# Performance work log

Measured on AMD Instinct MI355X. Metric: run time of the kernel, lower is better.

Reference implementation:

```python
import jax, jax.numpy as jnp
import numpy as np

BITS = 4
GROUPSIZE = 128
IN_FEATURES = 4096
OUT_FEATURES = 11008
PACK = 32 // BITS  # 8 nibbles per int32
MASK = (1 << BITS) - 1


def setup_inputs() -> dict:
    key = jax.random.key(0)
    k_x, k_qw, k_qz, k_s, k_b = jax.random.split(key, 5)
    n_groups = IN_FEATURES // GROUPSIZE  # 32
    x = jax.random.normal(k_x, (2, 2048, IN_FEATURES), dtype=jnp.float32)
    # packed int32 buffers: random bit patterns (each int32 holds 8 4-bit values)
    qweight = jax.random.randint(k_qw, (IN_FEATURES // 32 * BITS, OUT_FEATURES),
                                 -2**31, 2**31 - 1, dtype=jnp.int32)
    qzeros = jax.random.randint(k_qz, (n_groups, OUT_FEATURES // 32 * BITS),
                                -2**31, 2**31 - 1, dtype=jnp.int32)
    scales = jax.random.uniform(k_s, (n_groups, OUT_FEATURES), dtype=jnp.float32,
                                minval=0.001, maxval=0.02)
    bias = jax.random.normal(k_b, (OUT_FEATURES,), dtype=jnp.float32) * 0.01
    return {"x": x, "qweight": qweight, "scales": scales, "qzeros": qzeros, "bias": bias}


def _dequant(qweight, scales, qzeros):
    # shift amounts for each packed nibble: [0,4,...,28]
    wf = jnp.arange(0, 32, BITS, dtype=jnp.int32)
    n_groups = scales.shape[0]
    # unpack zeros: [G, out//8] -> [G, out//8, 8] -> [G, 1, out]
    zeros = jnp.bitwise_and(jnp.right_shift(qzeros[:, :, None], wf[None, None, :]), MASK)
    zeros = zeros.reshape(n_groups, 1, OUT_FEATURES).astype(scales.dtype)
    # unpack weights: [in//8, out] -> [in//8, 8, out] -> [G, groupsize, out]
    w = jnp.bitwise_and(jnp.right_shift(qweight[:, None, :], wf[None, :, None]), MASK)
    w = w.reshape(n_groups, GROUPSIZE, OUT_FEATURES).astype(scales.dtype)
    sc = scales[:, None, :]  # [G, 1, out]
    weight = sc * w - sc * zeros  # scales*w - scale_zeros
    return weight.reshape(IN_FEATURES, OUT_FEATURES)


def reference(x, qweight, scales, qzeros, bias):
    weight = _dequant(qweight, scales, qzeros)
    return jnp.matmul(x, weight) + bias
```

## Files before the change

### kernel.cpp

```cpp
#include <hip/hip_runtime.h>
#include <cstdint>
#include <cstddef>

#define IN_F 4096
#define OUT_F 11008
#define M_ROWS 4096
#define QZ_STRIDE (OUT_F / 8)
#define NKT (IN_F / 128)
#define NGROUPS 32

typedef __attribute__((ext_vector_type(4))) float f32x4;
typedef __attribute__((ext_vector_type(4))) int i32x4;
typedef __attribute__((ext_vector_type(8))) __bf16 bf16x8;
typedef uint32_t u32;
typedef uint16_t u16;
typedef uint8_t u8;

__device__ __forceinline__ u16 f2bf(float f) {
  u32 u = __builtin_bit_cast(u32, f);
  u += 0x7FFFu + ((u >> 16) & 1u);
  return (u16)(u >> 16);
}

__global__ __launch_bounds__(256) void conv_x_i8(const float* __restrict__ x,
                                                 u8* __restrict__ xq,
                                                 float* __restrict__ xs) {
  const int row = blockIdx.x;
  const int tid = threadIdx.x;
  const float* xr = x + (size_t)row * IN_F;
  float4 v[4];
#pragma unroll
  for (int j = 0; j < 4; ++j)
    v[j] = reinterpret_cast<const float4*>(xr)[tid * 4 + j];
  float am = 0.f;
#pragma unroll
  for (int j = 0; j < 4; ++j)
    am = fmaxf(am, fmaxf(fmaxf(fabsf(v[j].x), fabsf(v[j].y)),
                         fmaxf(fabsf(v[j].z), fabsf(v[j].w))));
#pragma unroll
  for (int off = 32; off > 0; off >>= 1) am = fmaxf(am, __shfl_xor(am, off, 64));
  __shared__ float wmax[4];
  if ((tid & 63) == 0) wmax[tid >> 6] = am;
  __syncthreads();
  am = fmaxf(fmaxf(wmax[0], wmax[1]), fmaxf(wmax[2], wmax[3]));
  const float amc = fmaxf(am, 1e-30f);
  const float inv = 127.f / amc;
  if (tid == 0) xs[row] = amc / 127.f;
  u32 o[4];
#pragma unroll
  for (int j = 0; j < 4; ++j) {
    u32 b0 = (u32)(u8)(int8_t)__float2int_rn(v[j].x * inv);
    u32 b1 = (u32)(u8)(int8_t)__float2int_rn(v[j].y * inv);
    u32 b2 = (u32)(u8)(int8_t)__float2int_rn(v[j].z * inv);
    u32 b3 = (u32)(u8)(int8_t)__float2int_rn(v[j].w * inv);
    o[j] = b0 | (b1 << 8) | (b2 << 16) | (b3 << 24);
  }
  *reinterpret_cast<uint4*>(xq + (size_t)row * IN_F + tid * 16) =
      make_uint4(o[0], o[1], o[2], o[3]);
}

__global__ void colscale_kernel(const float* __restrict__ scl,
                                float* __restrict__ Scol,
                                float* __restrict__ invScol) {
  const int n = blockIdx.x * 256 + threadIdx.x;
  if (n >= OUT_F) return;
  float m = 0.f;
#pragma unroll 4
  for (int g = 0; g < NGROUPS; ++g) m = fmaxf(m, scl[(size_t)g * OUT_F + n]);
  const float S = m * (15.f / 127.f);
  Scol[n] = S;
  invScol[n] = 1.f / S;
}

__global__ void dequant_i8(const int* __restrict__ qw, const int* __restrict__ qz,
                           const float* __restrict__ scl,
                           const float* __restrict__ invScol,
                           u8* __restrict__ wq8) {
  const int nl = threadIdx.x & 31, rl = threadIdx.x >> 5;
  const int n = blockIdx.x * 32 + nl;
  const int r = blockIdx.y * 8 + rl;
  const int g = r >> 4;
  u32 q = (u32)qw[(size_t)r * OUT_F + n];
  const int z = (int)(((u32)qz[g * QZ_STRIDE + (n >> 3)] >> (4 * (n & 7))) & 15u);
  const float si = scl[(size_t)g * OUT_F + n] * invScol[n];
  u32 lo = 0, hi = 0;
#pragma unroll
  for (int e = 0; e < 4; ++e) {
    float f = fminf(fmaxf((float)((int)((q >> (4 * e)) & 15u) - z) * si, -127.f), 127.f);
    lo |= ((u32)(u8)(int8_t)__float2int_rn(f)) << (8 * e);
  }
#pragma unroll
  for (int e = 0; e < 4; ++e) {
    float f = fminf(fmaxf((float)((int)((q >> (16 + 4 * e)) & 15u) - z) * si, -127.f), 127.f);
    hi |= ((u32)(u8)(int8_t)__float2int_rn(f)) << (8 * e);
  }
  *reinterpret_cast<uint2*>(wq8 + (size_t)n * IN_F + r * 8) = make_uint2(lo, hi);
}

__global__ __launch_bounds__(512, 2) void gemm256_i8(
    const u8* __restrict__ xq, const u8* __restrict__ wq,
    const float* __restrict__ Scol, const float* __restrict__ xs,
    const float* __restrict__ bias, float* __restrict__ out) {
  __shared__ __align__(16) u8 As[2][256 * 128];
  __shared__ __align__(16) u8 Bs[2][256 * 128];
  const int tid = threadIdx.x;
  const int lane = tid & 63, wid = tid >> 6;
  const int cpx = (int)gridDim.x >> 3;
  const int swz = ((int)blockIdx.x & 7) * cpx + ((int)blockIdx.x >> 3);
  const int m0 = (swz & 15) * 256, n0 = (swz >> 4) * 256;
  const int wr = wid >> 2, wc = wid & 3;
  const int frow = lane & 15, q4 = lane >> 4, f7 = lane & 7;
  const int lrow = lane >> 3, ls = lane & 7;

  const int colb0 = ((q4 ^ f7) << 4);
  const int colb1 = (((4 | q4) ^ f7) << 4);
  const int arowB = (wr * 128 + frow) * 128;
  const int browB = (wc * 64 + frow) * 128;

  const u8* gA = xq + (size_t)(m0 + lrow) * IN_F + ((ls ^ lrow) << 4);
  const u8* gB = wq + (size_t)(n0 + lrow) * IN_F + ((ls ^ lrow) << 4);
  const int rsbase = (wid >> 2) * 128 + (wid & 3) * 16;

  i32x4 acc[8][4] = {};
  i32x4 af[4][2], ah[4][2], bf[4][2];

  auto stage = [&](u8* ldsb, const u8* gl, int u, int h) {
#pragma unroll
    for (int j = 0; j < 2; ++j) {
      const int rowstart = rsbase + j * 8 + h * 64;
      __builtin_amdgcn_global_load_lds(
          (__attribute__((address_space(1))) void*)(gl + (size_t)rowstart * IN_F + (size_t)u * 128),
          (__attribute__((address_space(3))) void*)(ldsb + rowstart * 128), 16, 0, 0);
    }
  };

  stage(Bs[0], gB, 0, 0);
  stage(Bs[0], gB, 0, 1);
  stage(As[0], gA, 0, 0);
  stage(As[0], gA, 0, 1);
  stage(Bs[1], gB, 1, 0);
  stage(Bs[1], gB, 1, 1);
  stage(As[1], gA, 1, 0);
  stage(As[1], gA, 1, 1);
  asm volatile("s_waitcnt vmcnt(8)" ::: "memory");
  __builtin_amdgcn_s_barrier();
  {
    const u8* Ac = As[0];
    const u8* Bc = Bs[0];
#pragma unroll
    for (int ni = 0; ni < 4; ++ni) {
      bf[ni][0] = *reinterpret_cast<const i32x4*>(Bc + browB + ni * 2048 + colb0);
      bf[ni][1] = *reinterpret_cast<const i32x4*>(Bc + browB + ni * 2048 + colb1);
    }
#pragma unroll
    for (int mi = 0; mi < 4; ++mi) {
      af[mi][0] = *reinterpret_cast<const i32x4*>(Ac + arowB + mi * 2048 + colb0);
      af[mi][1] = *reinterpret_cast<const i32x4*>(Ac + arowB + mi * 2048 + colb1);
    }
  }

  for (int u = 0; u < NKT; ++u) {
    const int cur = u & 1;
    const u8* Ac = As[cur];
    const u8* An = As[cur ^ 1];
    const u8* Bn = Bs[cur ^ 1];
    const bool stT = (u + 2 < NKT);

    __builtin_amdgcn_s_barrier();
    asm volatile("s_waitcnt lgkmcnt(0)" ::: "memory");
    __builtin_amdgcn_sched_barrier(0);
    __builtin_amdgcn_s_setprio(1);
#pragma unroll
    for (int mi = 0; mi < 4; ++mi)
#pragma unroll
      for (int ni = 0; ni < 4; ++ni) {
        acc[mi][ni] = __builtin_amdgcn_mfma_i32_16x16x64_i8(af[mi][0], bf[ni][0], acc[mi][ni], 0, 0, 0);
        acc[mi][ni] = __builtin_amdgcn_mfma_i32_16x16x64_i8(af[mi][1], bf[ni][1], acc[mi][ni], 0, 0, 0);
      }
    __builtin_amdgcn_s_setprio(0);
    if (stT) {
      stage(Bs[cur], gB, u + 2, 0);
      stage(Bs[cur], gB, u + 2, 1);
    }
#pragma unroll
    for (int mi = 0; mi < 4; ++mi) {
      ah[mi][0] = *reinterpret_cast<const i32x4*>(Ac + arowB + (4 + mi) * 2048 + colb0);
      ah[mi][1] = *reinterpret_cast<const i32x4*>(Ac + arowB + (4 + mi) * 2048 + colb1);
    }

    __builtin_amdgcn_s_barrier();
    asm volatile("s_waitcnt lgkmcnt(0)" ::: "memory");
    __builtin_amdgcn_sched_barrier(0);
    __builtin_amdgcn_s_setprio(1);
#pragma unroll
    for (int mi = 0; mi < 4; ++mi)
#pragma unroll
      for (int ni = 0; ni < 4; ++ni) {
        acc[4 + mi][ni] = __builtin_amdgcn_mfma_i32_16x16x64_i8(ah[mi][0], bf[ni][0], acc[4 + mi][ni], 0, 0, 0);
        acc[4 + mi][ni] = __builtin_amdgcn_mfma_i32_16x16x64_i8(ah[mi][1], bf[ni][1], acc[4 + mi][ni], 0, 0, 0);
      }
    __builtin_amdgcn_s_setprio(0);
    if (stT) {
      stage(As[cur], gA, u + 2, 0);
      stage(As[cur], gA, u + 2, 1);
    }
    if (stT)
      asm volatile("s_waitcnt vmcnt(8)" ::: "memory");
    else
      asm volatile("s_waitcnt vmcnt(0)" ::: "memory");
    if (u + 1 < NKT) {
#pragma unroll
      for (int ni = 0; ni < 4; ++ni) {
        bf[ni][0] = *reinterpret_cast<const i32x4*>(Bn + browB + ni * 2048 + colb0);
        bf[ni][1] = *reinterpret_cast<const i32x4*>(Bn + browB + ni * 2048 + colb1);
      }
#pragma unroll
      for (int mi = 0; mi < 4; ++mi) {
        af[mi][0] = *reinterpret_cast<const i32x4*>(An + arowB + mi * 2048 + colb0);
        af[mi][1] = *reinterpret_cast<const i32x4*>(An + arowB + mi * 2048 + colb1);
      }
    }
  }

  const int crow = (lane >> 4) * 4, ccol = lane & 15;
#pragma unroll
  for (int mi = 0; mi < 8; ++mi) {
    const int rowb = m0 + wr * 128 + mi * 16 + crow;
    float sxv[4];
#pragma unroll
    for (int r2 = 0; r2 < 4; ++r2) sxv[r2] = xs[rowb + r2];
#pragma unroll
    for (int ni = 0; ni < 4; ++ni) {
      const int col = n0 + wc * 64 + ni * 16 + ccol;
      const float bv = bias[col];
      const float sv = Scol[col];
#pragma unroll
      for (int r2 = 0; r2 < 4; ++r2)
        __builtin_nontemporal_store(
            fmaf(sxv[r2] * sv, (float)acc[mi][ni][r2], bv),
            out + (size_t)(rowb + r2) * OUT_F + col);
    }
  }
}

__global__ __launch_bounds__(256, 2) void gemm_fused(
    const float* __restrict__ x, const int* __restrict__ qw,
    const int* __restrict__ qz, const float* __restrict__ sc,
    const float* __restrict__ bias, float* __restrict__ out) {
  __shared__ u16 Asb[128 * 64];
  __shared__ u16 Bsb[128 * 64];
  const int tid = threadIdx.x;
  const int lane = tid & 63, wid = tid >> 6;
  const int bm = blockIdx.x & 31, bn = blockIdx.x >> 5;
  const int m0 = bm * 128, n0 = bn * 128;
  const int wr = wid >> 1, wc = wid & 1;
  const int frow = lane & 15, fk = (lane >> 4) * 8;
  f32x4 acc[4][4] = {};

  for (int kt = 0; kt < 64; ++kt) {
    const int k0 = kt * 64;
#pragma unroll
    for (int it = 0; it < 8; ++it) {
      int c = it * 256 + tid;
      int row = c >> 4, c4 = c & 15;
      float4 v = *reinterpret_cast<const float4*>(
          x + (size_t)(m0 + row) * IN_F + k0 + c4 * 4);
      uint2 o;
      o.x = (u32)f2bf(v.x) | ((u32)f2bf(v.y) << 16);
      o.y = (u32)f2bf(v.z) | ((u32)f2bf(v.w) << 16);
      *reinterpret_cast<uint2*>(Asb + row * 64 + c4 * 4) = o;
    }
    {
      int nl = tid & 127, rq = tid >> 7;
      int n = n0 + nl;
      int gq = k0 >> 7;
      int z = (int)(((u32)qz[gq * QZ_STRIDE + (n >> 3)] >> (4 * (n & 7))) & 15u);
      float s = sc[gq * OUT_F + n];
#pragma unroll
      for (int j = 0; j < 4; ++j) {
        int r = (k0 >> 3) + rq * 4 + j;
        u32 q = (u32)qw[(size_t)r * OUT_F + n];
        u32 o[4];
#pragma unroll
        for (int e = 0; e < 4; ++e) {
          u16 lo = f2bf(s * (float)((int)((q >> (8 * e)) & 15u) - z));
          u16 hi = f2bf(s * (float)((int)((q >> (8 * e + 4)) & 15u) - z));
          o[e] = (u32)lo | ((u32)hi << 16);
        }
        *reinterpret_cast<uint4*>(Bsb + nl * 64 + (rq * 4 + j) * 8) =
            make_uint4(o[0], o[1], o[2], o[3]);
      }
    }
    __syncthreads();
#pragma unroll
    for (int kk = 0; kk < 64; kk += 32) {
      bf16x8 a[4], b[4];
#pragma unroll
      for (int mi = 0; mi < 4; ++mi)
        a[mi] = *reinterpret_cast<const bf16x8*>(Asb + (wr * 64 + mi * 16 + frow) * 64 + kk + fk);
#pragma unroll
      for (int ni = 0; ni < 4; ++ni)
        b[ni] = *reinterpret_cast<const bf16x8*>(Bsb + (wc * 64 + ni * 16 + frow) * 64 + kk + fk);
#pragma unroll
      for (int mi = 0; mi < 4; ++mi)
#pragma unroll
        for (int ni = 0; ni < 4; ++ni)
          acc[mi][ni] = __builtin_amdgcn_mfma_f32_16x16x32_bf16(a[mi], b[ni], acc[mi][ni], 0, 0, 0);
    }
    __syncthreads();
  }
  const int crow = (lane >> 4) * 4, ccol = lane & 15;
#pragma unroll
  for (int mi = 0; mi < 4; ++mi) {
#pragma unroll
    for (int ni = 0; ni < 4; ++ni) {
      int col = n0 + wc * 64 + ni * 16 + ccol;
      float bv = bias[col];
      int rowb = m0 + wr * 64 + mi * 16 + crow;
#pragma unroll
      for (int r2 = 0; r2 < 4; ++r2)
        out[(size_t)(rowb + r2) * OUT_F + col] = acc[mi][ni][r2] + bv;
    }
  }
}

extern "C" void kernel_launch(void* const* d_in, const int* in_sizes, int n_in,
                              void* d_out, int out_size, void* d_ws, size_t ws_size,
                              hipStream_t stream) {
  const float* x = (const float*)d_in[0];
  const int* qw = (const int*)d_in[1];
  const float* sc = (const float*)d_in[2];
  const int* qz = (const int*)d_in[3];
  const float* bias = (const float*)d_in[4];
  float* out = (float*)d_out;

  const size_t xq_bytes = (size_t)M_ROWS * IN_F;
  const size_t wq_bytes = (size_t)OUT_F * IN_F;
  const size_t xs_bytes = (size_t)M_ROWS * 4;
  const size_t sc_bytes = (size_t)OUT_F * 4;

  if (ws_size >= xq_bytes + wq_bytes + xs_bytes + 2 * sc_bytes) {
    u8* xqp = (u8*)d_ws;
    u8* wqp = (u8*)d_ws + xq_bytes;
    float* xsp = (float*)((u8*)d_ws + xq_bytes + wq_bytes);
    float* Scolp = (float*)((u8*)d_ws + xq_bytes + wq_bytes + xs_bytes);
    float* invScolp = Scolp + OUT_F;
    hipLaunchKernelGGL(conv_x_i8, dim3(M_ROWS), dim3(256), 0, stream, x, xqp, xsp);
    hipLaunchKernelGGL(colscale_kernel, dim3((OUT_F + 255) / 256), dim3(256), 0,
                       stream, sc, Scolp, invScolp);
    hipLaunchKernelGGL(dequant_i8, dim3(OUT_F / 32, 512 / 8), dim3(256), 0,
                       stream, qw, qz, sc, invScolp, wqp);
    hipLaunchKernelGGL(gemm256_i8, dim3((M_ROWS / 256) * (OUT_F / 256)),
                       dim3(512), 0, stream, xqp, wqp, Scolp, xsp, bias, out);
  } else {
    hipLaunchKernelGGL(gemm_fused, dim3(32 * 86), dim3(256), 0, stream, x, qw,
                       qz, sc, bias, out);
  }
}
```

Measured before the change: 248.8 us.

## Split int8 GEMM main loop into eight barrier-synchronized quadrant phases

Restructures the gemm256_i8 K-loop into eight small phases. Each phase runs one 2x2 quadrant of MFMAs, with LDS fragment reads and global-to-LDS prefetches interleaved between phases. Fragment registers shrink from full A/B sets to two small ping-pong buffers, and global pointers are precomputed and incremented instead of recomputed. The aim is finer overlap of LDS traffic, async loads and MFMA work, plus lower register pressure. The cost is many more barriers and waitcnt points per iteration, which can serialize the waves.

```diff
diff --git a/kernel.cpp b/kernel.cpp
--- a/kernel.cpp
+++ b/kernel.cpp
@@ -96,6 +96,48 @@
   }
   *reinterpret_cast<uint2*>(wq8 + (size_t)n * IN_F + r * 8) = make_uint2(lo, hi);
 }
+
+#define SP1 __builtin_amdgcn_s_setprio(1)
+#define SP0 __builtin_amdgcn_s_setprio(0)
+#define BAR __builtin_amdgcn_s_barrier()
+#define PH_SYNC()                                      \
+  __builtin_amdgcn_s_barrier();                        \
+  asm volatile("s_waitcnt lgkmcnt(0)" ::: "memory");   \
+  __builtin_amdgcn_sched_barrier(0)
+
+#define READ_A(ab, pair, base)                                                                  \
+  do {                                                                                          \
+    afr[ab][0][0] = *reinterpret_cast<const i32x4*>((base) + arowB + (2 * (pair)) * 2048 + colb0); \
+    afr[ab][0][1] = *reinterpret_cast<const i32x4*>((base) + arowB + (2 * (pair)) * 2048 + colb1); \
+    afr[ab][1][0] = *reinterpret_cast<const i32x4*>((base) + arowB + (2 * (pair) + 1) * 2048 + colb0); \
+    afr[ab][1][1] = *reinterpret_cast<const i32x4*>((base) + arowB + (2 * (pair) + 1) * 2048 + colb1); \
+  } while (0)
+
+#define READ_B(np, base)                                                                        \
+  do {                                                                                          \
+    bfr[np][0][0] = *reinterpret_cast<const i32x4*>((base) + browB + (2 * (np)) * 2048 + colb0); \
+    bfr[np][0][1] = *reinterpret_cast<const i32x4*>((base) + browB + (2 * (np)) * 2048 + colb1); \
+    bfr[np][1][0] = *reinterpret_cast<const i32x4*>((base) + browB + (2 * (np) + 1) * 2048 + colb0); \
+    bfr[np][1][1] = *reinterpret_cast<const i32x4*>((base) + browB + (2 * (np) + 1) * 2048 + colb1); \
+  } while (0)
+
+#define MFMA_Q(mp, np, ab)                                                                      \
+  do {                                                                                          \
+    SP1;                                                                                        \
+    _Pragma("unroll") for (int m = 0; m < 2; ++m)                                               \
+        _Pragma("unroll") for (int n = 0; n < 2; ++n) {                                         \
+      acc[2 * (mp) + m][2 * (np) + n] = __builtin_amdgcn_mfma_i32_16x16x64_i8(                  \
+          afr[ab][m][0], bfr[np][n][0], acc[2 * (mp) + m][2 * (np) + n], 0, 0, 0);              \
+      acc[2 * (mp) + m][2 * (np) + n] = __builtin_amdgcn_mfma_i32_16x16x64_i8(                  \
+          afr[ab][m][1], bfr[np][n][1], acc[2 * (mp) + m][2 * (np) + n], 0, 0, 0);              \
+    }                                                                                           \
+    SP0;                                                                                        \
+  } while (0)
+
+#define GLDS(gp, ldsoff)                                                            \
+  __builtin_amdgcn_global_load_lds(                                                 \
+      (__attribute__((address_space(1))) void*)(gp),                                \
+      (__attribute__((address_space(3))) void*)(ldsoff), 16, 0, 0)
 
 __global__ __launch_bounds__(512, 2) void gemm256_i8(
     const u8* __restrict__ xq, const u8* __restrict__ wq,
@@ -120,17 +162,17 @@
   const u8* gA = xq + (size_t)(m0 + lrow) * IN_F + ((ls ^ lrow) << 4);
   const u8* gB = wq + (size_t)(n0 + lrow) * IN_F + ((ls ^ lrow) << 4);
   const int rsbase = (wid >> 2) * 128 + (wid & 3) * 16;
+  const int r0 = rsbase, r1 = rsbase + 8, r2 = rsbase + 64, r3 = rsbase + 72;
+  const int o0 = r0 * 128, o1 = r1 * 128, o2 = r2 * 128, o3 = r3 * 128;
 
   i32x4 acc[8][4] = {};
-  i32x4 af[4][2], ah[4][2], bf[4][2];
+  i32x4 afr[2][2][2], bfr[2][2][2];
 
   auto stage = [&](u8* ldsb, const u8* gl, int u, int h) {
 #pragma unroll
     for (int j = 0; j < 2; ++j) {
       const int rowstart = rsbase + j * 8 + h * 64;
-      __builtin_amdgcn_global_load_lds(
-          (__attribute__((address_space(1))) void*)(gl + (size_t)rowstart * IN_F + (size_t)u * 128),
-          (__attribute__((address_space(3))) void*)(ldsb + rowstart * 128), 16, 0, 0);
+      GLDS(gl + (size_t)rowstart * IN_F + (size_t)u * 128, ldsb + rowstart * 128);
     }
   };
 
@@ -144,82 +186,78 @@
   stage(As[1], gA, 1, 1);
   asm volatile("s_waitcnt vmcnt(8)" ::: "memory");
   __builtin_amdgcn_s_barrier();
-  {
-    const u8* Ac = As[0];
-    const u8* Bc = Bs[0];
-#pragma unroll
-    for (int ni = 0; ni < 4; ++ni) {
-      bf[ni][0] = *reinterpret_cast<const i32x4*>(Bc + browB + ni * 2048 + colb0);
-      bf[ni][1] = *reinterpret_cast<const i32x4*>(Bc + browB + ni * 2048 + colb1);
-    }
-#pragma unroll
-    for (int mi = 0; mi < 4; ++mi) {
-      af[mi][0] = *reinterpret_cast<const i32x4*>(Ac + arowB + mi * 2048 + colb0);
-      af[mi][1] = *reinterpret_cast<const i32x4*>(Ac + arowB + mi * 2048 + colb1);
-    }
-  }
+  READ_A(0, 0, (const u8*)As[0]);
+  READ_B(0, (const u8*)Bs[0]);
+
+  const u8* pA0 = gA + (size_t)r0 * IN_F + 256;
+  const u8* pA1 = gA + (size_t)r1 * IN_F + 256;
+  const u8* pA2 = gA + (size_t)r2 * IN_F + 256;
+  const u8* pA3 = gA + (size_t)r3 * IN_F + 256;
+  const u8* pB0 = gB + (size_t)r0 * IN_F + 256;
+  const u8* pB1 = gB + (size_t)r1 * IN_F + 256;
+  const u8* pB2 = gB + (size_t)r2 * IN_F + 256;
+  const u8* pB3 = gB + (size_t)r3 * IN_F + 256;
 
   for (int u = 0; u < NKT; ++u) {
     const int cur = u & 1;
-    const u8* Ac = As[cur];
-    const u8* An = As[cur ^ 1];
-    const u8* Bn = Bs[cur ^ 1];
+    const u8* Ac = (const u8*)As[cur];
+    const u8* Bc = (const u8*)Bs[cur];
+    const u8* An = (const u8*)As[cur ^ 1];
+    const u8* Bn = (const u8*)Bs[cur ^ 1];
+    u8* Ast = (u8*)As[cur];
+    u8* Bst = (u8*)Bs[cur];
     const bool stT = (u + 2 < NKT);
 
-    __builtin_amdgcn_s_barrier();
-    asm volatile("s_waitcnt lgkmcnt(0)" ::: "memory");
-    __builtin_amdgcn_sched_barrier(0);
-    __builtin_amdgcn_s_setprio(1);
-#pragma unroll
-    for (int mi = 0; mi < 4; ++mi)
-#pragma unroll
-      for (int ni = 0; ni < 4; ++ni) {
-        acc[mi][ni] = __builtin_amdgcn_mfma_i32_16x16x64_i8(af[mi][0], bf[ni][0], acc[mi][ni], 0, 0, 0);
-        acc[mi][ni] = __builtin_amdgcn_mfma_i32_16x16x64_i8(af[mi][1], bf[ni][1], acc[mi][ni], 0, 0, 0);
-      }
-    __builtin_amdgcn_s_setprio(0);
-    if (stT) {
-      stage(Bs[cur], gB, u + 2, 0);
-      stage(Bs[cur], gB, u + 2, 1);
-    }
-#pragma unroll
-    for (int mi = 0; mi < 4; ++mi) {
-      ah[mi][0] = *reinterpret_cast<const i32x4*>(Ac + arowB + (4 + mi) * 2048 + colb0);
-      ah[mi][1] = *reinterpret_cast<const i32x4*>(Ac + arowB + (4 + mi) * 2048 + colb1);
-    }
-
-    __builtin_amdgcn_s_barrier();
-    asm volatile("s_waitcnt lgkmcnt(0)" ::: "memory");
-    __builtin_amdgcn_sched_barrier(0);
-    __builtin_amdgcn_s_setprio(1);
-#pragma unroll
-    for (int mi = 0; mi < 4; ++mi)
-#pragma unroll
-      for (int ni = 0; ni < 4; ++ni) {
-        acc[4 + mi][ni] = __builtin_amdgcn_mfma_i32_16x16x64_i8(ah[mi][0], bf[ni][0], acc[4 + mi][ni], 0, 0, 0);
-        acc[4 + mi][ni] = __builtin_amdgcn_mfma_i32_16x16x64_i8(ah[mi][1], bf[ni][1], acc[4 + mi][ni], 0, 0, 0);
-      }
-    __builtin_amdgcn_s_setprio(0);
-    if (stT) {
-      stage(As[cur], gA, u + 2, 0);
-      stage(As[cur], gA, u + 2, 1);
-    }
+    READ_B(1, Bc);
+    PH_SYNC();
+    MFMA_Q(0, 0, 0);
+    BAR;
+
+    READ_A(1, 1, Ac);
+    PH_SYNC();
+    MFMA_Q(0, 1, 0);
+    BAR;
+
+    if (stT) { GLDS(pB0, Bst + o0); GLDS(pB1, Bst + o1); }
+    PH_SYNC();
+    MFMA_Q(1, 1, 1);
+    BAR;
+
+    READ_A(0, 2, Ac);
+    if (stT) { GLDS(pB2, Bst + o2); GLDS(pB3, Bst + o3); }
+    PH_SYNC();
+    MFMA_Q(1, 0, 1);
+    BAR;
+
+    READ_A(1, 3, Ac);
+    PH_SYNC();
+    MFMA_Q(2, 0, 0);
+    BAR;
+
+    if (stT) { GLDS(pA0, Ast + o0); GLDS(pA1, Ast + o1); }
+    PH_SYNC();
+    MFMA_Q(2, 1, 0);
+    BAR;
+
+    if (stT) { GLDS(pA2, Ast + o2); GLDS(pA3, Ast + o3); }
+    PH_SYNC();
+    MFMA_Q(3, 0, 1);
+    BAR;
+
     if (stT)
       asm volatile("s_waitcnt vmcnt(8)" ::: "memory");
     else
       asm volatile("s_waitcnt vmcnt(0)" ::: "memory");
     if (u + 1 < NKT) {
-#pragma unroll
-      for (int ni = 0; ni < 4; ++ni) {
-        bf[ni][0] = *reinterpret_cast<const i32x4*>(Bn + browB + ni * 2048 + colb0);
-        bf[ni][1] = *reinterpret_cast<const i32x4*>(Bn + browB + ni * 2048 + colb1);
-      }
-#pragma unroll
-      for (int mi = 0; mi < 4; ++mi) {
-        af[mi][0] = *reinterpret_cast<const i32x4*>(An + arowB + mi * 2048 + colb0);
-        af[mi][1] = *reinterpret_cast<const i32x4*>(An + arowB + mi * 2048 + colb1);
-      }
-    }
+      READ_A(0, 0, An);
+      READ_B(0, Bn);
+    }
+    PH_SYNC();
+    MFMA_Q(3, 1, 1);
+    BAR;
+
+    pA0 += 128; pA1 += 128; pA2 += 128; pA3 += 128;
+    pB0 += 128; pB1 += 128; pB2 += 128; pB3 += 128;
   }
 
   const int crow = (lane >> 4) * 4, ccol = lane & 15;
@@ -228,17 +266,17 @@
     const int rowb = m0 + wr * 128 + mi * 16 + crow;
     float sxv[4];
 #pragma unroll
-    for (int r2 = 0; r2 < 4; ++r2) sxv[r2] = xs[rowb + r2];
+    for (int r5 = 0; r5 < 4; ++r5) sxv[r5] = xs[rowb + r5];
 #pragma unroll
     for (int ni = 0; ni < 4; ++ni) {
       const int col = n0 + wc * 64 + ni * 16 + ccol;
       const float bv = bias[col];
       const float sv = Scol[col];
 #pragma unroll
-      for (int r2 = 0; r2 < 4; ++r2)
+      for (int r5 = 0; r5 < 4; ++r5)
         __builtin_nontemporal_store(
-            fmaf(sxv[r2] * sv, (float)acc[mi][ni][r2], bv),
-            out + (size_t)(rowb + r2) * OUT_F + col);
+            fmaf(sxv[r5] * sv, (float)acc[mi][ni][r5], bv),
+            out + (size_t)(rowb + r5) * OUT_F + col);
     }
   }
 }
@@ -318,8 +356,8 @@
       float bv = bias[col];
       int rowb = m0 + wr * 64 + mi * 16 + crow;
 #pragma unroll
-      for (int r2 = 0; r2 < 4; ++r2)
-        out[(size_t)(rowb + r2) * OUT_F + col] = acc[mi][ni][r2] + bv;
+      for (int r5 = 0; r5 < 4; ++r5)
+        out[(size_t)(rowb + r5) * OUT_F + col] = acc[mi][ni][r5] + bv;
     }
   }
 }
```

Result: slower. 261.5 us (+5.1%).

## Pre-swizzle int8 operands into MFMA fragment layout and load straight to registers

Applied to the files above, without the earlier changes.

The quantize and dequant kernels now write x and the weights in a tiled layout that matches the MFMA 16x64 fragment order. The GEMM drops shared memory and the global_load_lds staging, and each wave loads fragments directly from global memory into registers, with double-buffered register sets. The block tile shrinks from 256x256 to 256x128 and each wave computes a 64x64 tile. This removes LDS traffic and barriers, but operands are no longer shared through LDS, so more global/L2 traffic is redundant and there is less reuse per block.

```diff
diff --git a/kernel.cpp b/kernel.cpp
--- a/kernel.cpp
+++ b/kernel.cpp
@@ -8,6 +8,7 @@
 #define QZ_STRIDE (OUT_F / 8)
 #define NKT (IN_F / 128)
 #define NGROUPS 32
+#define KC (IN_F / 64)
 
 typedef __attribute__((ext_vector_type(4))) float f32x4;
 typedef __attribute__((ext_vector_type(4))) int i32x4;
@@ -23,7 +24,7 @@
 }
 
 __global__ __launch_bounds__(256) void conv_x_i8(const float* __restrict__ x,
-                                                 u8* __restrict__ xq,
+                                                 u8* __restrict__ xqf,
                                                  float* __restrict__ xs) {
   const int row = blockIdx.x;
   const int tid = threadIdx.x;
@@ -55,8 +56,10 @@
     u32 b3 = (u32)(u8)(int8_t)__float2int_rn(v[j].w * inv);
     o[j] = b0 | (b1 << 8) | (b2 << 16) | (b3 << 24);
   }
-  *reinterpret_cast<uint4*>(xq + (size_t)row * IN_F + tid * 16) =
-      make_uint4(o[0], o[1], o[2], o[3]);
+  const int k0 = tid * 16;
+  u8* dst = xqf + ((size_t)(row >> 4) * KC + (k0 >> 6)) * 1024 +
+            (size_t)(((row & 15) + (((k0 >> 4) & 3) << 4)) * 16);
+  *reinterpret_cast<uint4*>(dst) = make_uint4(o[0], o[1], o[2], o[3]);
 }
 
 __global__ void colscale_kernel(const float* __restrict__ scl,
@@ -75,7 +78,7 @@
 __global__ void dequant_i8(const int* __restrict__ qw, const int* __restrict__ qz,
                            const float* __restrict__ scl,
                            const float* __restrict__ invScol,
-                           u8* __restrict__ wq8) {
+                           u8* __restrict__ wqf) {
   const int nl = threadIdx.x & 31, rl = threadIdx.x >> 5;
   const int n = blockIdx.x * 32 + nl;
   const int r = blockIdx.y * 8 + rl;
@@ -94,138 +97,74 @@
     float f = fminf(fmaxf((float)((int)((q >> (16 + 4 * e)) & 15u) - z) * si, -127.f), 127.f);
     hi |= ((u32)(u8)(int8_t)__float2int_rn(f)) << (8 * e);
   }
-  *reinterpret_cast<uint2*>(wq8 + (size_t)n * IN_F + r * 8) = make_uint2(lo, hi);
-}
-
-__global__ __launch_bounds__(512, 2) void gemm256_i8(
-    const u8* __restrict__ xq, const u8* __restrict__ wq,
+  const int k0 = r * 8;
+  u8* dst = wqf + ((size_t)(n >> 4) * KC + (k0 >> 6)) * 1024 +
+            (size_t)(((n & 15) + (((k0 >> 4) & 3) << 4)) * 16) + (k0 & 8);
+  *reinterpret_cast<uint2*>(dst) = make_uint2(lo, hi);
+}
+
+__global__ __launch_bounds__(512, 2) void gemm_reg_i8(
+    const u8* __restrict__ xqf, const u8* __restrict__ wqf,
     const float* __restrict__ Scol, const float* __restrict__ xs,
     const float* __restrict__ bias, float* __restrict__ out) {
-  __shared__ __align__(16) u8 As[2][256 * 128];
-  __shared__ __align__(16) u8 Bs[2][256 * 128];
   const int tid = threadIdx.x;
   const int lane = tid & 63, wid = tid >> 6;
   const int cpx = (int)gridDim.x >> 3;
   const int swz = ((int)blockIdx.x & 7) * cpx + ((int)blockIdx.x >> 3);
-  const int m0 = (swz & 15) * 256, n0 = (swz >> 4) * 256;
-  const int wr = wid >> 2, wc = wid & 3;
-  const int frow = lane & 15, q4 = lane >> 4, f7 = lane & 7;
-  const int lrow = lane >> 3, ls = lane & 7;
-
-  const int colb0 = ((q4 ^ f7) << 4);
-  const int colb1 = (((4 | q4) ^ f7) << 4);
-  const int arowB = (wr * 128 + frow) * 128;
-  const int browB = (wc * 64 + frow) * 128;
-
-  const u8* gA = xq + (size_t)(m0 + lrow) * IN_F + ((ls ^ lrow) << 4);
-  const u8* gB = wq + (size_t)(n0 + lrow) * IN_F + ((ls ^ lrow) << 4);
-  const int rsbase = (wid >> 2) * 128 + (wid & 3) * 16;
-
-  i32x4 acc[8][4] = {};
-  i32x4 af[4][2], ah[4][2], bf[4][2];
-
-  auto stage = [&](u8* ldsb, const u8* gl, int u, int h) {
-#pragma unroll
-    for (int j = 0; j < 2; ++j) {
-      const int rowstart = rsbase + j * 8 + h * 64;
-      __builtin_amdgcn_global_load_lds(
-          (__attribute__((address_space(1))) void*)(gl + (size_t)rowstart * IN_F + (size_t)u * 128),
-          (__attribute__((address_space(3))) void*)(ldsb + rowstart * 128), 16, 0, 0);
-    }
-  };
-
-  stage(Bs[0], gB, 0, 0);
-  stage(Bs[0], gB, 0, 1);
-  stage(As[0], gA, 0, 0);
-  stage(As[0], gA, 0, 1);
-  stage(Bs[1], gB, 1, 0);
-  stage(Bs[1], gB, 1, 1);
-  stage(As[1], gA, 1, 0);
-  stage(As[1], gA, 1, 1);
-  asm volatile("s_waitcnt vmcnt(8)" ::: "memory");
-  __builtin_amdgcn_s_barrier();
-  {
-    const u8* Ac = As[0];
-    const u8* Bc = Bs[0];
-#pragma unroll
-    for (int ni = 0; ni < 4; ++ni) {
-      bf[ni][0] = *reinterpret_cast<const i32x4*>(Bc + browB + ni * 2048 + colb0);
-      bf[ni][1] = *reinterpret_cast<const i32x4*>(Bc + browB + ni * 2048 + colb1);
-    }
-#pragma unroll
-    for (int mi = 0; mi < 4; ++mi) {
-      af[mi][0] = *reinterpret_cast<const i32x4*>(Ac + arowB + mi * 2048 + colb0);
-      af[mi][1] = *reinterpret_cast<const i32x4*>(Ac + arowB + mi * 2048 + colb1);
-    }
-  }
-
-  for (int u = 0; u < NKT; ++u) {
-    const int cur = u & 1;
-    const u8* Ac = As[cur];
-    const u8* An = As[cur ^ 1];
-    const u8* Bn = Bs[cur ^ 1];
-    const bool stT = (u + 2 < NKT);
-
-    __builtin_amdgcn_s_barrier();
-    asm volatile("s_waitcnt lgkmcnt(0)" ::: "memory");
-    __builtin_amdgcn_sched_barrier(0);
-    __builtin_amdgcn_s_setprio(1);
-#pragma unroll
-    for (int mi = 0; mi < 4; ++mi)
-#pragma unroll
-      for (int ni = 0; ni < 4; ++ni) {
-        acc[mi][ni] = __builtin_amdgcn_mfma_i32_16x16x64_i8(af[mi][0], bf[ni][0], acc[mi][ni], 0, 0, 0);
-        acc[mi][ni] = __builtin_amdgcn_mfma_i32_16x16x64_i8(af[mi][1], bf[ni][1], acc[mi][ni], 0, 0, 0);
-      }
-    __builtin_amdgcn_s_setprio(0);
-    if (stT) {
-      stage(Bs[cur], gB, u + 2, 0);
-      stage(Bs[cur], gB, u + 2, 1);
-    }
-#pragma unroll
-    for (int mi = 0; mi < 4; ++mi) {
-      ah[mi][0] = *reinterpret_cast<const i32x4*>(Ac + arowB + (4 + mi) * 2048 + colb0);
-      ah[mi][1] = *reinterpret_cast<const i32x4*>(Ac + arowB + (4 + mi) * 2048 + colb1);
-    }
-
-    __builtin_amdgcn_s_barrier();
-    asm volatile("s_waitcnt lgkmcnt(0)" ::: "memory");
-    __builtin_amdgcn_sched_barrier(0);
-    __builtin_amdgcn_s_setprio(1);
-#pragma unroll
-    for (int mi = 0; mi < 4; ++mi)
-#pragma unroll
-      for (int ni = 0; ni < 4; ++ni) {
-        acc[4 + mi][ni] = __builtin_amdgcn_mfma_i32_16x16x64_i8(ah[mi][0], bf[ni][0], acc[4 + mi][ni], 0, 0, 0);
-        acc[4 + mi][ni] = __builtin_amdgcn_mfma_i32_16x16x64_i8(ah[mi][1], bf[ni][1], acc[4 + mi][ni], 0, 0, 0);
-      }
-    __builtin_amdgcn_s_setprio(0);
-    if (stT) {
-      stage(As[cur], gA, u + 2, 0);
-      stage(As[cur], gA, u + 2, 1);
-    }
-    if (stT)
-      asm volatile("s_waitcnt vmcnt(8)" ::: "memory");
-    else
-      asm volatile("s_waitcnt vmcnt(0)" ::: "memory");
-    if (u + 1 < NKT) {
-#pragma unroll
-      for (int ni = 0; ni < 4; ++ni) {
-        bf[ni][0] = *reinterpret_cast<const i32x4*>(Bn + browB + ni * 2048 + colb0);
-        bf[ni][1] = *reinterpret_cast<const i32x4*>(Bn + browB + ni * 2048 + colb1);
-      }
-#pragma unroll
-      for (int mi = 0; mi < 4; ++mi) {
-        af[mi][0] = *reinterpret_cast<const i32x4*>(An + arowB + mi * 2048 + colb0);
-        af[mi][1] = *reinterpret_cast<const i32x4*>(An + arowB + mi * 2048 + colb1);
-      }
-    }
+  const int mIdx = swz & 15, nIdx = swz >> 4;
+  const int m0 = mIdx * 256, n0 = nIdx * 128;
+  const int wr = wid >> 1, wc = wid & 1;
+
+  const u8* pa[4];
+  const u8* pb[4];
+#pragma unroll
+  for (int mi = 0; mi < 4; ++mi)
+    pa[mi] = xqf + ((size_t)((m0 >> 4) + wr * 4 + mi) * KC) * 1024 + lane * 16;
+#pragma unroll
+  for (int ni = 0; ni < 4; ++ni)
+    pb[ni] = wqf + ((size_t)((n0 >> 4) + wc * 4 + ni) * KC) * 1024 + lane * 16;
+
+  i32x4 a0[4][2], b0[4][2], a1[4][2], b1[4][2];
+  i32x4 acc[4][4] = {};
+
+#define LOADT(A, B, u)                                                        \
+  do {                                                                        \
+    const int _off = (u) * 2048;                                              \
+    _Pragma("unroll") for (int mi = 0; mi < 4; ++mi) {                        \
+      A[mi][0] = *reinterpret_cast<const i32x4*>(pa[mi] + _off);              \
+      A[mi][1] = *reinterpret_cast<const i32x4*>(pa[mi] + _off + 1024);       \
+    }                                                                         \
+    _Pragma("unroll") for (int ni = 0; ni < 4; ++ni) {                        \
+      B[ni][0] = *reinterpret_cast<const i32x4*>(pb[ni] + _off);              \
+      B[ni][1] = *reinterpret_cast<const i32x4*>(pb[ni] + _off + 1024);       \
+    }                                                                         \
+  } while (0)
+
+#define MFMAT(A, B)                                                           \
+  do {                                                                        \
+    __builtin_amdgcn_s_setprio(1);                                            \
+    _Pragma("unroll") for (int mi = 0; mi < 4; ++mi)                          \
+        _Pragma("unroll") for (int ni = 0; ni < 4; ++ni) {                    \
+      acc[mi][ni] = __builtin_amdgcn_mfma_i32_16x16x64_i8(                    \
+          A[mi][0], B[ni][0], acc[mi][ni], 0, 0, 0);                          \
+      acc[mi][ni] = __builtin_amdgcn_mfma_i32_16x16x64_i8(                    \
+          A[mi][1], B[ni][1], acc[mi][ni], 0, 0, 0);                          \
+    }                                                                         \
+    __builtin_amdgcn_s_setprio(0);                                            \
+  } while (0)
+
+  LOADT(a0, b0, 0);
+  for (int u = 0; u < NKT; u += 2) {
+    if (u + 1 < NKT) LOADT(a1, b1, u + 1);
+    MFMAT(a0, b0);
+    if (u + 2 < NKT) LOADT(a0, b0, u + 2);
+    if (u + 1 < NKT) MFMAT(a1, b1);
   }
 
   const int crow = (lane >> 4) * 4, ccol = lane & 15;
 #pragma unroll
-  for (int mi = 0; mi < 8; ++mi) {
-    const int rowb = m0 + wr * 128 + mi * 16 + crow;
+  for (int mi = 0; mi < 4; ++mi) {
+    const int rowb = m0 + wr * 64 + mi * 16 + crow;
     float sxv[4];
 #pragma unroll
     for (int r2 = 0; r2 < 4; ++r2) sxv[r2] = xs[rowb + r2];
@@ -350,7 +289,7 @@
                        stream, sc, Scolp, invScolp);
     hipLaunchKernelGGL(dequant_i8, dim3(OUT_F / 32, 512 / 8), dim3(256), 0,
                        stream, qw, qz, sc, invScolp, wqp);
-    hipLaunchKernelGGL(gemm256_i8, dim3((M_ROWS / 256) * (OUT_F / 256)),
+    hipLaunchKernelGGL(gemm_reg_i8, dim3((M_ROWS / 256) * (OUT_F / 128)),
                        dim3(512), 0, stream, xqp, wqp, Scolp, xsp, bias, out);
   } else {
     hipLaunchKernelGGL(gemm_fused, dim3(32 * 86), dim3(256), 0, stream, x, qw,
```

Measured after the change: 295.5 us. 18.7% more time.

## Stage GEMM epilogue through LDS for coalesced stores and remap tiles per XCD

Applied to the files above, without the earlier changes.

Merges the A and B LDS buffers into one shared array so it can be reused after the main loop. The epilogue now writes scaled results into LDS in two halves, then each wave stores full 1KB rows with 16-byte vectors instead of scattered 4-byte stores. The block-to-tile mapping changes so each XCD handles two adjacent M tiles across all N tiles, aiming for better L2 reuse of A. This adds extra barriers and LDS traffic in the epilogue.

```diff
diff --git a/kernel.cpp b/kernel.cpp
--- a/kernel.cpp
+++ b/kernel.cpp
@@ -97,17 +97,21 @@
   *reinterpret_cast<uint2*>(wq8 + (size_t)n * IN_F + r * 8) = make_uint2(lo, hi);
 }
 
+#define ASB(i) (SMEM + ((i) << 15))
+#define BSB(i) (SMEM + 65536 + ((i) << 15))
+
 __global__ __launch_bounds__(512, 2) void gemm256_i8(
     const u8* __restrict__ xq, const u8* __restrict__ wq,
     const float* __restrict__ Scol, const float* __restrict__ xs,
     const float* __restrict__ bias, float* __restrict__ out) {
-  __shared__ __align__(16) u8 As[2][256 * 128];
-  __shared__ __align__(16) u8 Bs[2][256 * 128];
+  __shared__ __align__(16) u8 SMEM[131072];
   const int tid = threadIdx.x;
   const int lane = tid & 63, wid = tid >> 6;
-  const int cpx = (int)gridDim.x >> 3;
-  const int swz = ((int)blockIdx.x & 7) * cpx + ((int)blockIdx.x >> 3);
-  const int m0 = (swz & 15) * 256, n0 = (swz >> 4) * 256;
+  const int xcd = (int)blockIdx.x & 7;
+  const int l = (int)blockIdx.x >> 3;
+  const int mIdx = xcd * 2 + (l & 1);
+  const int nIdx = l >> 1;
+  const int m0 = mIdx * 256, n0 = nIdx * 256;
   const int wr = wid >> 2, wc = wid & 3;
   const int frow = lane & 15, q4 = lane >> 4, f7 = lane & 7;
   const int lrow = lane >> 3, ls = lane & 7;
@@ -134,19 +138,19 @@
     }
   };
 
-  stage(Bs[0], gB, 0, 0);
-  stage(Bs[0], gB, 0, 1);
-  stage(As[0], gA, 0, 0);
-  stage(As[0], gA, 0, 1);
-  stage(Bs[1], gB, 1, 0);
-  stage(Bs[1], gB, 1, 1);
-  stage(As[1], gA, 1, 0);
-  stage(As[1], gA, 1, 1);
+  stage(BSB(0), gB, 0, 0);
+  stage(BSB(0), gB, 0, 1);
+  stage(ASB(0), gA, 0, 0);
+  stage(ASB(0), gA, 0, 1);
+  stage(BSB(1), gB, 1, 0);
+  stage(BSB(1), gB, 1, 1);
+  stage(ASB(1), gA, 1, 0);
+  stage(ASB(1), gA, 1, 1);
   asm volatile("s_waitcnt vmcnt(8)" ::: "memory");
   __builtin_amdgcn_s_barrier();
   {
-    const u8* Ac = As[0];
-    const u8* Bc = Bs[0];
+    const u8* Ac = ASB(0);
+    const u8* Bc = BSB(0);
 #pragma unroll
     for (int ni = 0; ni < 4; ++ni) {
       bf[ni][0] = *reinterpret_cast<const i32x4*>(Bc + browB + ni * 2048 + colb0);
@@ -161,9 +165,9 @@
 
   for (int u = 0; u < NKT; ++u) {
     const int cur = u & 1;
-    const u8* Ac = As[cur];
-    const u8* An = As[cur ^ 1];
-    const u8* Bn = Bs[cur ^ 1];
+    const u8* Ac = ASB(cur);
+    const u8* An = ASB(cur ^ 1);
+    const u8* Bn = BSB(cur ^ 1);
     const bool stT = (u + 2 < NKT);
 
     __builtin_amdgcn_s_barrier();
@@ -179,8 +183,8 @@
       }
     __builtin_amdgcn_s_setprio(0);
     if (stT) {
-      stage(Bs[cur], gB, u + 2, 0);
-      stage(Bs[cur], gB, u + 2, 1);
+      stage(BSB(cur), gB, u + 2, 0);
+      stage(BSB(cur), gB, u + 2, 1);
     }
 #pragma unroll
     for (int mi = 0; mi < 4; ++mi) {
@@ -201,8 +205,8 @@
       }
     __builtin_amdgcn_s_setprio(0);
     if (stT) {
-      stage(As[cur], gA, u + 2, 0);
-      stage(As[cur], gA, u + 2, 1);
+      stage(ASB(cur), gA, u + 2, 0);
+      stage(ASB(cur), gA, u + 2, 1);
     }
     if (stT)
       asm volatile("s_waitcnt vmcnt(8)" ::: "memory");
@@ -222,23 +226,38 @@
     }
   }
 
+  float* cs = reinterpret_cast<float*>(SMEM);
   const int crow = (lane >> 4) * 4, ccol = lane & 15;
 #pragma unroll
-  for (int mi = 0; mi < 8; ++mi) {
-    const int rowb = m0 + wr * 128 + mi * 16 + crow;
-    float sxv[4];
-#pragma unroll
-    for (int r2 = 0; r2 < 4; ++r2) sxv[r2] = xs[rowb + r2];
-#pragma unroll
-    for (int ni = 0; ni < 4; ++ni) {
-      const int col = n0 + wc * 64 + ni * 16 + ccol;
-      const float bv = bias[col];
-      const float sv = Scol[col];
-#pragma unroll
-      for (int r2 = 0; r2 < 4; ++r2)
-        __builtin_nontemporal_store(
-            fmaf(sxv[r2] * sv, (float)acc[mi][ni][r2], bv),
-            out + (size_t)(rowb + r2) * OUT_F + col);
+  for (int p = 0; p < 2; ++p) {
+    __syncthreads();
+    if (wr == p) {
+#pragma unroll
+      for (int mi = 0; mi < 8; ++mi) {
+        const int rl = mi * 16 + crow;
+        const int rowg = m0 + p * 128 + rl;
+        float sxv[4];
+#pragma unroll
+        for (int r2 = 0; r2 < 4; ++r2) sxv[r2] = xs[rowg + r2];
+#pragma unroll
+        for (int ni = 0; ni < 4; ++ni) {
+          const int col = wc * 64 + ni * 16 + ccol;
+          const float sv = Scol[n0 + col];
+          const float bv = bias[n0 + col];
+#pragma unroll
+          for (int r2 = 0; r2 < 4; ++r2)
+            cs[(rl + r2) * 256 + col] =
+                fmaf(sxv[r2] * sv, (float)acc[mi][ni][r2], bv);
+        }
+      }
+    }
+    __syncthreads();
+#pragma unroll
+    for (int rr = 0; rr < 16; ++rr) {
+      const int r = wid * 16 + rr;
+      f32x4 v = *reinterpret_cast<const f32x4*>(cs + r * 256 + lane * 4);
+      __builtin_nontemporal_store(
+          v, reinterpret_cast<f32x4*>(out + (size_t)(m0 + p * 128 + r) * OUT_F + n0 + lane * 4));
     }
   }
 }
```

After: 212.5 us. -14.6%, faster.
